# Kernel optimization log

Measured on AMD Instinct MI355X. Metric: run time of the kernel, lower is better.

The kernel has to match this reference:

```python
import jax, jax.numpy as jnp
import numpy as np

B, L, T = 256, 256, 50  # batch, max_len, num_tags


def setup_inputs() -> dict:
    key = jax.random.key(0)
    k1, k2, k3 = jax.random.split(key, 3)
    feats = jax.random.normal(k1, (B, L, T), dtype=jnp.float32)
    trans_m = jax.random.normal(k2, (T, T), dtype=jnp.float32)
    tags = jax.random.randint(k3, (B, L), 0, T)
    mask = jnp.ones((B, L), dtype=jnp.int32)
    return {"feats": feats, "trans_m": trans_m, "tags": tags, "mask": mask}


def _normalizer(logits, trans_m, m):
    # logits: (L, B, T), m: (L, B) float mask
    alpha0 = logits[0]  # (B, T)

    def step(alpha, inp):
        emit, mt = inp  # (B, T), (B,)
        # (B, T_from, T_to) broadcast add, logsumexp over T_from
        tmp = alpha[:, :, None] + trans_m[None, :, :] + emit[:, None, :]
        new = jax.nn.logsumexp(tmp, axis=1)
        alpha = jnp.where(mt[:, None] > 0, new, alpha)
        return alpha, None

    alpha, _ = jax.lax.scan(step, alpha0, (logits[1:], m[1:]))
    return jax.nn.logsumexp(alpha, axis=1)  # (B,)


def _gold_score(logits, trans_m, tags_t, m):
    # logits: (L, B, T); tags_t: (L, B); m: (L, B)
    trans_sc = trans_m[tags_t[:-1], tags_t[1:]] * m[1:]  # (L-1, B)
    emit_sc = jnp.take_along_axis(logits, tags_t[:, :, None], axis=2)[..., 0] * m  # (L, B)
    return jnp.sum(trans_sc + emit_sc[:-1], axis=0) + emit_sc[-1]  # (B,)


def reference(feats, trans_m, tags, mask):
    # feats: (B, L, T) -> (L, B, T); include_start_end_trans=False
    logits = jnp.transpose(feats, (1, 0, 2))
    tags_t = tags.T
    m = mask.T.astype(feats.dtype)
    all_path = _normalizer(logits, trans_m, m)
    gold = _gold_score(logits, trans_m, tags_t, m)
    return all_path - gold  # (B,) loss per example
```

## Files before the change

### kernel.cpp

```cpp
#include <hip/hip_runtime.h>
#include <math.h>


#define TAGS 50
#define LEN 256
#define NB 256
#define TOTF (NB * LEN * TAGS)
#define INV_LN2 1.4426950408889634f
#define LN2 0.6931471805599453f

typedef __attribute__((ext_vector_type(8))) short bf16x8;
typedef __attribute__((ext_vector_type(4))) float f32x4;
typedef __attribute__((ext_vector_type(4), aligned(4))) float f32x4u;

#if __has_builtin(__builtin_amdgcn_exp2f)
#define EXP2F(x) __builtin_amdgcn_exp2f(x)
#else
#define EXP2F(x) exp2f(x)
#endif
#if __has_builtin(__builtin_amdgcn_logf)
#define LOG2F(x) __builtin_amdgcn_logf(x)
#else
#define LOG2F(x) log2f(x)
#endif
#if __has_builtin(__builtin_amdgcn_rcpf)
#define RCPF(x) __builtin_amdgcn_rcpf(x)
#else
#define RCPF(x) (1.0f / (x))
#endif

__device__ __forceinline__ float readlane_f(float v, int srclane) {
  return __builtin_bit_cast(float,
      __builtin_amdgcn_readlane(__builtin_bit_cast(int, v), srclane));
}

__device__ __forceinline__ int bf16pairInit(float lo, float hi) {
  unsigned lb = (__builtin_bit_cast(unsigned, lo) + 0x8000u) >> 16;
  unsigned hb = (__builtin_bit_cast(unsigned, hi) + 0x8000u) & 0xFFFF0000u;
  return (int)(hb | lb);
}

#define PACK2(dst, lo, hi) \
  asm("v_cvt_pk_bf16_f32 %0, %1, %2" : "=v"(dst) : "v"(lo), "v"(hi))

union U8 { int i[4]; bf16x8 v; };

#define WS_U(b)  ((b) * 64)
#define WS_W(b)  ((NB + (b)) * 64)
#define WS_SF(b) (2 * NB * 64 + (b))
#define WS_SB(b) (2 * NB * 64 + NB + (b))

__global__ __launch_bounds__(512, 1) void crf_seg_kernel(
    const float* __restrict__ feats,
    const float* __restrict__ trans,
    const int*   __restrict__ mask,
    float*       __restrict__ ws)
{
  const int bid    = blockIdx.x;
  const bool is_fwd = bid < NB;
  const int b      = is_fwd ? bid : bid - NB;
  const int tid    = threadIdx.x;
  const int w      = tid >> 6;
  const int lane   = tid & 63;
  const int q      = lane >> 4;
  const int n      = lane & 15;

  __shared__ __align__(16) float x_lds[64];
  __shared__ float Sseg[8];

  const int* mbp = mask + b * LEN;
  const unsigned long long mb0 = __ballot(mbp[lane] > 0);
  const unsigned long long mb1 = __ballot(mbp[64 + lane] > 0);
  const unsigned long long mb2 = __ballot(mbp[128 + lane] > 0);
  const unsigned long long mb3 = __ballot(mbp[192 + lane] > 0);
#define MASKBIT(L)                                                          \
  ((int)(((((L) & 128) ? (((L) & 64) ? mb3 : mb2)                           \
                       : (((L) & 64) ? mb1 : mb0)) >> ((L) & 63)) & 1ull))

  U8 Afr[4][2];
#pragma unroll
  for (int t = 0; t < 4; ++t)
#pragma unroll
    for (int c = 0; c < 2; ++c)
#pragma unroll
      for (int r = 0; r < 4; ++r) {
        const int col = 16 * t + n;
        const int tag0 = 16 * c + 4 * q + r;
        const int tag1 = tag0 + 32;
        float e0 = 0.0f, e1 = 0.0f;
        if (col < TAGS) {
          if (tag0 < TAGS)
            e0 = EXP2F((is_fwd ? trans[tag0 * TAGS + col]
                               : trans[col * TAGS + tag0]) * INV_LN2);
          if (tag1 < TAGS)
            e1 = EXP2F((is_fwd ? trans[tag1 * TAGS + col]
                               : trans[col * TAGS + tag1]) * INV_LN2);
        }
        Afr[t][c].i[r] = bf16pairInit(e0, e1);
      }

  const f32x4 zero4 = {0.0f, 0.0f, 0.0f, 0.0f};

  f32x4 d[4][4];
#pragma unroll
  for (int J = 0; J < 4; ++J)
#pragma unroll
    for (int I = 0; I < 4; ++I)
#pragma unroll
      for (int r = 0; r < 4; ++r)
        d[J][I][r] = (16 * J + n == 16 * I + 4 * q + r) ? 1.0f : 0.0f;

  float S = 0.0f;
  f32x4u rA[4], rB[4];

#define LOADG(BK, L) do {                                                   \
    const float* _p = feats + (size_t)b * (LEN * TAGS) + (size_t)(L) * TAGS;\
    BK[0] = *(const f32x4u*)(_p + 4 * q);                                   \
    BK[1] = *(const f32x4u*)(_p + 16 + 4 * q);                              \
    BK[2] = *(const f32x4u*)(_p + 32 + 4 * q);                              \
    const float* _p3 = _p + 46 + 4 * q;                                     \
    const float* _lim = feats + (TOTF - 4);                                 \
    if (_p3 > _lim) _p3 = _lim;                                             \
    BK[3] = *(const f32x4u*)_p3;                                            \
  } while (0)

#define RENORMM() do {                                                      \
    const float _cc = readlane_f(d[0][0][0], 0);                            \
    const float _rr = RCPF(_cc);                                            \
    S += LOG2F(_cc);                                                        \
    _Pragma("unroll") for (int _J = 0; _J < 4; ++_J)                        \
    _Pragma("unroll") for (int _I = 0; _I < 4; ++_I)                        \
    _Pragma("unroll") for (int _r = 0; _r < 4; ++_r)                        \
      d[_J][_I][_r] *= _rr;                                                 \
  } while (0)

#define MKEV(EH)                                                            \
    float ev[4][4];                                                         \
    _Pragma("unroll") for (int _i = 0; _i < 3; ++_i)                        \
    _Pragma("unroll") for (int _r = 0; _r < 4; ++_r)                        \
      ev[_i][_r] = EXP2F(EH[_i][_r] * INV_LN2);                             \
    ev[3][0] = EXP2F(EH[3][2] * INV_LN2);                                   \
    ev[3][1] = EXP2F(EH[3][3] * INV_LN2);                                   \
    ev[3][2] = 0.0f; ev[3][3] = 0.0f

#define MFMA8J(B0_, B1_)                                                    \
    f32x4 t0 = __builtin_amdgcn_mfma_f32_16x16x32_bf16(Afr[0][1].v, B1_.v, zero4, 0, 0, 0); \
    f32x4 t1 = __builtin_amdgcn_mfma_f32_16x16x32_bf16(Afr[1][1].v, B1_.v, zero4, 0, 0, 0); \
    f32x4 t2 = __builtin_amdgcn_mfma_f32_16x16x32_bf16(Afr[2][1].v, B1_.v, zero4, 0, 0, 0); \
    f32x4 t3 = __builtin_amdgcn_mfma_f32_16x16x32_bf16(Afr[3][1].v, B1_.v, zero4, 0, 0, 0); \
    t0 = __builtin_amdgcn_mfma_f32_16x16x32_bf16(Afr[0][0].v, B0_.v, t0, 0, 0, 0); \
    t1 = __builtin_amdgcn_mfma_f32_16x16x32_bf16(Afr[1][0].v, B0_.v, t1, 0, 0, 0); \
    t2 = __builtin_amdgcn_mfma_f32_16x16x32_bf16(Afr[2][0].v, B0_.v, t2, 0, 0, 0); \
    t3 = __builtin_amdgcn_mfma_f32_16x16x32_bf16(Afr[3][0].v, B0_.v, t3, 0, 0, 0)

#define STEPF(EH, L) do {                                                   \
    if ((L) <= 127 && MASKBIT(L)) {                                         \
      MKEV(EH);                                                             \
      _Pragma("unroll") for (int _J = 0; _J < 4; ++_J) {                    \
        U8 B0, B1;                                                          \
        _Pragma("unroll") for (int _r = 0; _r < 4; ++_r) {                  \
          PACK2(B0.i[_r], d[_J][0][_r], d[_J][2][_r]);                      \
          PACK2(B1.i[_r], d[_J][1][_r], d[_J][3][_r]);                      \
        }                                                                   \
        MFMA8J(B0, B1);                                                     \
        _Pragma("unroll") for (int _r = 0; _r < 4; ++_r) {                  \
          d[_J][0][_r] = t0[_r] * ev[0][_r];                                \
          d[_J][1][_r] = t1[_r] * ev[1][_r];                                \
          d[_J][2][_r] = t2[_r] * ev[2][_r];                                \
          d[_J][3][_r] = t3[_r] * ev[3][_r];                                \
        }                                                                   \
      }                                                                     \
    }                                                                       \
  } while (0)

#define STEPB(EH, L) do {                                                   \
    if (MASKBIT(L)) {                                                       \
      MKEV(EH);                                                             \
      _Pragma("unroll") for (int _J = 0; _J < 4; ++_J) {                    \
        U8 B0, B1;                                                          \
        _Pragma("unroll") for (int _r = 0; _r < 4; ++_r) {                  \
          PACK2(B0.i[_r], ev[0][_r] * d[_J][0][_r], ev[2][_r] * d[_J][2][_r]); \
          PACK2(B1.i[_r], ev[1][_r] * d[_J][1][_r], ev[3][_r] * d[_J][3][_r]); \
        }                                                                   \
        MFMA8J(B0, B1);                                                     \
        _Pragma("unroll") for (int _r = 0; _r < 4; ++_r) {                  \
          d[_J][0][_r] = t0[_r];                                            \
          d[_J][1][_r] = t1[_r];                                            \
          d[_J][2][_r] = t2[_r];                                            \
          d[_J][3][_r] = t3[_r];                                            \
        }                                                                   \
      }                                                                     \
    }                                                                       \
  } while (0)

  if (is_fwd) {
    int l = 1 + 16 * w;
    LOADG(rA, l);
    LOADG(rB, l + 1);
    for (int kk = 0; kk < 8; ++kk) {
      if ((kk & 1) == 0) RENORMM();
      STEPF(rA, l); LOADG(rA, l + 2);
      ++l;
      STEPF(rB, l); LOADG(rB, l + 2);
      ++l;
    }
  } else {
    int l = 143 + 16 * w;
    LOADG(rA, l);
    LOADG(rB, l - 1);
    for (int kk = 0; kk < 8; ++kk) {
      if ((kk & 1) == 0) RENORMM();
      STEPB(rA, l); LOADG(rA, l - 2);
      --l;
      STEPB(rB, l); LOADG(rB, l - 2);
      --l;
    }
  }

  __syncthreads();

  if (is_fwd) {
    for (int f = 0; f < 8; ++f) {
      if (w == f) {
        float xv[4];
        if (f == 0) {
#pragma unroll
          for (int J = 0; J < 4; ++J) {
            const int tg = 16 * J + n;
            xv[J] = (tg < TAGS)
                        ? EXP2F(feats[(size_t)b * (LEN * TAGS) + tg] * INV_LN2)
                        : 0.0f;
          }
        } else {
#pragma unroll
          for (int J = 0; J < 4; ++J) xv[J] = x_lds[16 * J + n];
        }
        float p[4][4];
#pragma unroll
        for (int I = 0; I < 4; ++I)
#pragma unroll
          for (int r = 0; r < 4; ++r)
            p[I][r] = xv[0] * d[0][I][r] + xv[1] * d[1][I][r] +
                      xv[2] * d[2][I][r] + xv[3] * d[3][I][r];
#pragma unroll
        for (int off = 1; off <= 8; off <<= 1)
#pragma unroll
          for (int I = 0; I < 4; ++I)
#pragma unroll
            for (int r = 0; r < 4; ++r)
              p[I][r] += __shfl_xor(p[I][r], off, 64);
        const float cc = readlane_f(p[0][0], 0);
        const float rr = RCPF(cc);
        S += LOG2F(cc);
        if (n == 0) {
#pragma unroll
          for (int I = 0; I < 4; ++I)
#pragma unroll
            for (int r = 0; r < 4; ++r)
              x_lds[16 * I + 4 * q + r] = p[I][r] * rr;
        }
        if (lane == 0) Sseg[w] = S;
      }
      __syncthreads();
    }
    if (tid < 64) ws[WS_U(b) + tid] = x_lds[tid];
    if (tid == 0) {
      float s = 0.0f;
#pragma unroll
      for (int i = 0; i < 8; ++i) s += Sseg[i];
      ws[WS_SF(b)] = s;
    }
  } else {
    for (int f2 = 0; f2 < 8; ++f2) {
      if (w == 7 - f2) {
        float xv[4];
        if (w == 7) {
#pragma unroll
          for (int J = 0; J < 4; ++J) xv[J] = (16 * J + n < TAGS) ? 1.0f : 0.0f;
        } else {
#pragma unroll
          for (int J = 0; J < 4; ++J) xv[J] = x_lds[16 * J + n];
        }
        float t[4][4];
#pragma unroll
        for (int I = 0; I < 4; ++I)
#pragma unroll
          for (int r = 0; r < 4; ++r)
            t[I][r] = xv[0] * d[0][I][r] + xv[1] * d[1][I][r] +
                      xv[2] * d[2][I][r] + xv[3] * d[3][I][r];
#pragma unroll
        for (int off = 1; off <= 8; off <<= 1)
#pragma unroll
          for (int I = 0; I < 4; ++I)
#pragma unroll
            for (int r = 0; r < 4; ++r)
              t[I][r] += __shfl_xor(t[I][r], off, 64);
        const float cc = readlane_f(t[0][0], 0);
        const float rr = RCPF(cc);
        S += LOG2F(cc);
        if (n == 0) {
#pragma unroll
          for (int I = 0; I < 4; ++I)
#pragma unroll
            for (int r = 0; r < 4; ++r)
              x_lds[16 * I + 4 * q + r] = t[I][r] * rr;
        }
        if (lane == 0) Sseg[w] = S;
      }
      __syncthreads();
    }
    if (tid < 64) ws[WS_W(b) + tid] = x_lds[tid];
    if (tid == 0) {
      float s = 0.0f;
#pragma unroll
      for (int i = 0; i < 8; ++i) s += Sseg[i];
      ws[WS_SB(b)] = s;
    }
  }
#undef MASKBIT
#undef LOADG
#undef RENORMM
#undef MKEV
#undef MFMA8J
#undef STEPF
#undef STEPB
}

__global__ __launch_bounds__(64) void crf_combine_kernel(
    const float* __restrict__ feats,
    const float* __restrict__ trans,
    const int*   __restrict__ tags,
    const int*   __restrict__ mask,
    const float* __restrict__ ws,
    float*       __restrict__ out)
{
  const int b = blockIdx.x;
  const int lane = threadIdx.x;

  float s = ws[WS_U(b) + lane] * ws[WS_W(b) + lane];
#pragma unroll
  for (int off = 32; off; off >>= 1) s += __shfl_xor(s, off, 64);

  const float* fb = feats + (size_t)b * (LEN * TAGS);
  const int*   tb = tags + b * LEN;
  const int*   mb = mask + b * LEN;
  float gp = 0.0f;
#pragma unroll
  for (int k = 0; k < 4; ++k) {
    const int p = lane + 64 * k;
    const int tg = tb[p];
    if (mb[p] > 0) {
      float vv = fb[p * TAGS + tg];
      if (p >= 1) vv += trans[tb[p - 1] * TAGS + tg];
      gp += vv;
    }
  }
#pragma unroll
  for (int off = 32; off; off >>= 1) gp += __shfl_xor(gp, off, 64);

  if (lane == 0) {
    const float Sf = ws[WS_SF(b)];
    const float Sb = ws[WS_SB(b)];
    out[b] = LN2 * (Sf + Sb + LOG2F(s)) - gp;
  }
}

extern "C" void kernel_launch(void* const* d_in, const int* in_sizes, int n_in,
                              void* d_out, int out_size, void* d_ws, size_t ws_size,
                              hipStream_t stream) {
  const float* feats = (const float*)d_in[0];
  const float* trans = (const float*)d_in[1];
  const int*   tags  = (const int*)d_in[2];
  const int*   mask  = (const int*)d_in[3];
  float* out = (float*)d_out;
  float* ws  = (float*)d_ws;

  crf_seg_kernel<<<2 * NB, 512, 0, stream>>>(feats, trans, mask, ws);
  crf_combine_kernel<<<NB, 64, 0, stream>>>(feats, trans, tags, mask, ws, out);
}
```

Measured before the change: 126.5 us.

## Fuse forward/backward segment blocks and combine kernel into one 1024-thread block

```diff
diff --git a/kernel.cpp b/kernel.cpp
--- a/kernel.cpp
+++ b/kernel.cpp
@@ -45,28 +45,26 @@
 
 union U8 { int i[4]; bf16x8 v; };
 
-#define WS_U(b)  ((b) * 64)
-#define WS_W(b)  ((NB + (b)) * 64)
-#define WS_SF(b) (2 * NB * 64 + (b))
-#define WS_SB(b) (2 * NB * 64 + NB + (b))
-
-__global__ __launch_bounds__(512, 1) void crf_seg_kernel(
+__global__ __launch_bounds__(1024, 1) void crf_fused_kernel(
     const float* __restrict__ feats,
     const float* __restrict__ trans,
+    const int*   __restrict__ tags,
     const int*   __restrict__ mask,
-    float*       __restrict__ ws)
+    float*       __restrict__ out)
 {
-  const int bid    = blockIdx.x;
-  const bool is_fwd = bid < NB;
-  const int b      = is_fwd ? bid : bid - NB;
-  const int tid    = threadIdx.x;
-  const int w      = tid >> 6;
-  const int lane   = tid & 63;
-  const int q      = lane >> 4;
-  const int n      = lane & 15;
-
-  __shared__ __align__(16) float x_lds[64];
-  __shared__ float Sseg[8];
+  const int b    = blockIdx.x;
+  const int tid  = threadIdx.x;
+  const int w    = tid >> 6;
+  const int lane = tid & 63;
+  const int q    = lane >> 4;
+  const int n    = lane & 15;
+  const bool isf = (w < 8);
+  const int  sw  = isf ? w : w - 8;
+
+  __shared__ __align__(16) float xf_lds[64];
+  __shared__ __align__(16) float xb_lds[64];
+  __shared__ float Sseg[16];
+  __shared__ float norm_s, gold_s;
 
   const int* mbp = mask + b * LEN;
   const unsigned long long mb0 = __ballot(mbp[lane] > 0);
@@ -90,11 +88,11 @@
         float e0 = 0.0f, e1 = 0.0f;
         if (col < TAGS) {
           if (tag0 < TAGS)
-            e0 = EXP2F((is_fwd ? trans[tag0 * TAGS + col]
-                               : trans[col * TAGS + tag0]) * INV_LN2);
+            e0 = EXP2F((isf ? trans[tag0 * TAGS + col]
+                            : trans[col * TAGS + tag0]) * INV_LN2);
           if (tag1 < TAGS)
-            e1 = EXP2F((is_fwd ? trans[tag1 * TAGS + col]
-                               : trans[col * TAGS + tag1]) * INV_LN2);
+            e1 = EXP2F((isf ? trans[tag1 * TAGS + col]
+                            : trans[col * TAGS + tag1]) * INV_LN2);
         }
         Afr[t][c].i[r] = bf16pairInit(e0, e1);
       }
@@ -193,8 +191,8 @@
     }                                                                       \
   } while (0)
 
-  if (is_fwd) {
-    int l = 1 + 16 * w;
+  if (isf) {
+    int l = 1 + 16 * sw;
     LOADG(rA, l);
     LOADG(rB, l + 1);
     for (int kk = 0; kk < 8; ++kk) {
@@ -205,7 +203,7 @@
       ++l;
     }
   } else {
-    int l = 143 + 16 * w;
+    int l = 143 + 16 * sw;
     LOADG(rA, l);
     LOADG(rB, l - 1);
     for (int kk = 0; kk < 8; ++kk) {
@@ -219,104 +217,117 @@
 
   __syncthreads();
 
-  if (is_fwd) {
-    for (int f = 0; f < 8; ++f) {
-      if (w == f) {
-        float xv[4];
-        if (f == 0) {
-#pragma unroll
-          for (int J = 0; J < 4; ++J) {
-            const int tg = 16 * J + n;
-            xv[J] = (tg < TAGS)
-                        ? EXP2F(feats[(size_t)b * (LEN * TAGS) + tg] * INV_LN2)
-                        : 0.0f;
-          }
-        } else {
-#pragma unroll
-          for (int J = 0; J < 4; ++J) xv[J] = x_lds[16 * J + n];
+  for (int f = 0; f < 8; ++f) {
+    if (w == f) {
+      float xv[4];
+      if (f == 0) {
+#pragma unroll
+        for (int J = 0; J < 4; ++J) {
+          const int tg = 16 * J + n;
+          xv[J] = (tg < TAGS)
+                      ? EXP2F(feats[(size_t)b * (LEN * TAGS) + tg] * INV_LN2)
+                      : 0.0f;
         }
-        float p[4][4];
+      } else {
+#pragma unroll
+        for (int J = 0; J < 4; ++J) xv[J] = xf_lds[16 * J + n];
+      }
+      float p[4][4];
+#pragma unroll
+      for (int I = 0; I < 4; ++I)
+#pragma unroll
+        for (int r = 0; r < 4; ++r)
+          p[I][r] = xv[0] * d[0][I][r] + xv[1] * d[1][I][r] +
+                    xv[2] * d[2][I][r] + xv[3] * d[3][I][r];
+#pragma unroll
+      for (int off = 1; off <= 8; off <<= 1)
 #pragma unroll
         for (int I = 0; I < 4; ++I)
 #pragma unroll
           for (int r = 0; r < 4; ++r)
-            p[I][r] = xv[0] * d[0][I][r] + xv[1] * d[1][I][r] +
-                      xv[2] * d[2][I][r] + xv[3] * d[3][I][r];
-#pragma unroll
-        for (int off = 1; off <= 8; off <<= 1)
-#pragma unroll
-          for (int I = 0; I < 4; ++I)
-#pragma unroll
-            for (int r = 0; r < 4; ++r)
-              p[I][r] += __shfl_xor(p[I][r], off, 64);
-        const float cc = readlane_f(p[0][0], 0);
-        const float rr = RCPF(cc);
-        S += LOG2F(cc);
-        if (n == 0) {
-#pragma unroll
-          for (int I = 0; I < 4; ++I)
-#pragma unroll
-            for (int r = 0; r < 4; ++r)
-              x_lds[16 * I + 4 * q + r] = p[I][r] * rr;
-        }
-        if (lane == 0) Sseg[w] = S;
-      }
-      __syncthreads();
-    }
-    if (tid < 64) ws[WS_U(b) + tid] = x_lds[tid];
-    if (tid == 0) {
-      float s = 0.0f;
-#pragma unroll
-      for (int i = 0; i < 8; ++i) s += Sseg[i];
-      ws[WS_SF(b)] = s;
-    }
-  } else {
-    for (int f2 = 0; f2 < 8; ++f2) {
-      if (w == 7 - f2) {
-        float xv[4];
-        if (w == 7) {
-#pragma unroll
-          for (int J = 0; J < 4; ++J) xv[J] = (16 * J + n < TAGS) ? 1.0f : 0.0f;
-        } else {
-#pragma unroll
-          for (int J = 0; J < 4; ++J) xv[J] = x_lds[16 * J + n];
-        }
-        float t[4][4];
+            p[I][r] += __shfl_xor(p[I][r], off, 64);
+      const float cc = readlane_f(p[0][0], 0);
+      const float rr = RCPF(cc);
+      S += LOG2F(cc);
+      if (n == 0) {
 #pragma unroll
         for (int I = 0; I < 4; ++I)
 #pragma unroll
           for (int r = 0; r < 4; ++r)
-            t[I][r] = xv[0] * d[0][I][r] + xv[1] * d[1][I][r] +
-                      xv[2] * d[2][I][r] + xv[3] * d[3][I][r];
-#pragma unroll
-        for (int off = 1; off <= 8; off <<= 1)
-#pragma unroll
-          for (int I = 0; I < 4; ++I)
-#pragma unroll
-            for (int r = 0; r < 4; ++r)
-              t[I][r] += __shfl_xor(t[I][r], off, 64);
-        const float cc = readlane_f(t[0][0], 0);
-        const float rr = RCPF(cc);
-        S += LOG2F(cc);
-        if (n == 0) {
-#pragma unroll
-          for (int I = 0; I < 4; ++I)
-#pragma unroll
-            for (int r = 0; r < 4; ++r)
-              x_lds[16 * I + 4 * q + r] = t[I][r] * rr;
-        }
-        if (lane == 0) Sseg[w] = S;
-      }
-      __syncthreads();
-    }
-    if (tid < 64) ws[WS_W(b) + tid] = x_lds[tid];
-    if (tid == 0) {
-      float s = 0.0f;
-#pragma unroll
-      for (int i = 0; i < 8; ++i) s += Sseg[i];
-      ws[WS_SB(b)] = s;
-    }
+            xf_lds[16 * I + 4 * q + r] = p[I][r] * rr;
+      }
+      if (lane == 0) Sseg[w] = S;
+    }
+    if (w == 8 + (7 - f)) {
+      float xv[4];
+      if (f == 0) {
+#pragma unroll
+        for (int J = 0; J < 4; ++J) xv[J] = (16 * J + n < TAGS) ? 1.0f : 0.0f;
+      } else {
+#pragma unroll
+        for (int J = 0; J < 4; ++J) xv[J] = xb_lds[16 * J + n];
+      }
+      float t[4][4];
+#pragma unroll
+      for (int I = 0; I < 4; ++I)
+#pragma unroll
+        for (int r = 0; r < 4; ++r)
+          t[I][r] = xv[0] * d[0][I][r] + xv[1] * d[1][I][r] +
+                    xv[2] * d[2][I][r] + xv[3] * d[3][I][r];
+#pragma unroll
+      for (int off = 1; off <= 8; off <<= 1)
+#pragma unroll
+        for (int I = 0; I < 4; ++I)
+#pragma unroll
+          for (int r = 0; r < 4; ++r)
+            t[I][r] += __shfl_xor(t[I][r], off, 64);
+      const float cc = readlane_f(t[0][0], 0);
+      const float rr = RCPF(cc);
+      S += LOG2F(cc);
+      if (n == 0) {
+#pragma unroll
+        for (int I = 0; I < 4; ++I)
+#pragma unroll
+          for (int r = 0; r < 4; ++r)
+            xb_lds[16 * I + 4 * q + r] = t[I][r] * rr;
+      }
+      if (lane == 0) Sseg[w] = S;
+    }
+    __syncthreads();
   }
+
+  if (w == 0) {
+    float s = xf_lds[lane] * xb_lds[lane];
+#pragma unroll
+    for (int off = 32; off; off >>= 1) s += __shfl_xor(s, off, 64);
+    if (lane == 0) {
+      float Ssum = 0.0f;
+#pragma unroll
+      for (int i = 0; i < 16; ++i) Ssum += Sseg[i];
+      norm_s = LN2 * (Ssum + LOG2F(s));
+    }
+  } else if (w == 1) {
+    const float* fb = feats + (size_t)b * (LEN * TAGS);
+    const int* tb = tags + b * LEN;
+    float gp = 0.0f;
+#pragma unroll
+    for (int k = 0; k < 4; ++k) {
+      const int p = lane + 64 * k;
+      const int tg = tb[p];
+      if (mbp[p] > 0) {
+        float vv = fb[p * TAGS + tg];
+        if (p >= 1) vv += trans[tb[p - 1] * TAGS + tg];
+        gp += vv;
+      }
+    }
+#pragma unroll
+    for (int off = 32; off; off >>= 1) gp += __shfl_xor(gp, off, 64);
+    if (lane == 0) gold_s = gp;
+  }
+
+  __syncthreads();
+  if (tid == 0) out[b] = norm_s - gold_s;
+
 #undef MASKBIT
 #undef LOADG
 #undef RENORMM
@@ -326,45 +337,6 @@
 #undef STEPB
 }
 
-__global__ __launch_bounds__(64) void crf_combine_kernel(
-    const float* __restrict__ feats,
-    const float* __restrict__ trans,
-    const int*   __restrict__ tags,
-    const int*   __restrict__ mask,
-    const float* __restrict__ ws,
-    float*       __restrict__ out)
-{
-  const int b = blockIdx.x;
-  const int lane = threadIdx.x;
-
-  float s = ws[WS_U(b) + lane] * ws[WS_W(b) + lane];
-#pragma unroll
-  for (int off = 32; off; off >>= 1) s += __shfl_xor(s, off, 64);
-
-  const float* fb = feats + (size_t)b * (LEN * TAGS);
-  const int*   tb = tags + b * LEN;
-  const int*   mb = mask + b * LEN;
-  float gp = 0.0f;
-#pragma unroll
-  for (int k = 0; k < 4; ++k) {
-    const int p = lane + 64 * k;
-    const int tg = tb[p];
-    if (mb[p] > 0) {
-      float vv = fb[p * TAGS + tg];
-      if (p >= 1) vv += trans[tb[p - 1] * TAGS + tg];
-      gp += vv;
-    }
-  }
-#pragma unroll
-  for (int off = 32; off; off >>= 1) gp += __shfl_xor(gp, off, 64);
-
-  if (lane == 0) {
-    const float Sf = ws[WS_SF(b)];
-    const float Sb = ws[WS_SB(b)];
-    out[b] = LN2 * (Sf + Sb + LOG2F(s)) - gp;
-  }
-}
-
 extern "C" void kernel_launch(void* const* d_in, const int* in_sizes, int n_in,
                               void* d_out, int out_size, void* d_ws, size_t ws_size,
                               hipStream_t stream) {
@@ -373,8 +345,7 @@
   const int*   tags  = (const int*)d_in[2];
   const int*   mask  = (const int*)d_in[3];
   float* out = (float*)d_out;
-  float* ws  = (float*)d_ws;
-
-  crf_seg_kernel<<<2 * NB, 512, 0, stream>>>(feats, trans, mask, ws);
-  crf_combine_kernel<<<NB, 64, 0, stream>>>(feats, trans, tags, mask, ws, out);
+  (void)d_ws; (void)ws_size;
+
+  crf_fused_kernel<<<NB, 1024, 0, stream>>>(feats, trans, tags, mask, out);
 }
```

Result: slower. 286.1 us (+126.2%).
